# Performance work log

Measured on AMD Instinct MI355X. Metric: run time of the kernel, lower is better.

Reference implementation:

```python
import jax, jax.numpy as jnp
import numpy as np

H, W = 256, 256
BLOCK_SIZES = [16, 1024, 1024, 24]


def get_binary_position_encoding(shape):
    # Per-pixel binary encoding of the (row, col) coordinates, MSB-first.
    encs = []
    for d in shape:
        nb = int(np.ceil(np.log2(d)))
        bits = (jnp.arange(d)[:, None] >> jnp.arange(nb - 1, -1, -1)[None, :]) & 1
        encs.append(bits.astype(bool))
    a = jnp.broadcast_to(encs[0][:, None, :], (shape[0], shape[1], encs[0].shape[-1]))
    b = jnp.broadcast_to(encs[1][None, :, :], (shape[0], shape[1], encs[1].shape[-1]))
    return jnp.concatenate([a, b], axis=-1)  # (H, W, 16) bool


def block_forward(x, mask, thr):
    # Original: expand x to (N, dim_in, dim_out), XNOR with mask, sum over dim_in,
    # threshold. XNOR-popcount == #{i : x[n,i] == mask[i,o]}, computed here as two
    # GEMMs without materializing the (N, dim_in, dim_out) intermediate.
    xf = x.astype(jnp.float32)
    mf = mask.astype(jnp.float32)
    sums = xf @ mf + (1.0 - xf) @ (1.0 - mf)  # exact integer counts in fp32
    return sums > thr.astype(jnp.float32)[None, :]


def bits_to_int(x):
    # (..., 8) bool bits, MSB-first -> int
    weights = (2 ** jnp.arange(7, -1, -1)).astype(jnp.int32)
    return jnp.sum(x.astype(jnp.int32) * weights, axis=-1)


def setup_inputs() -> dict:
    key = jax.random.key(0)
    ks = jax.random.split(key, 7)
    inp = {"image": jax.random.uniform(ks[0], (3, H, W), jnp.float32) * 255.0}
    for i, (di, do) in enumerate(zip(BLOCK_SIZES[:-1], BLOCK_SIZES[1:])):
        inp[f"mask{i}"] = jax.random.uniform(ks[1 + 2 * i], (di, do)) < 0.5
        inp[f"thr{i}"] = jax.random.randint(ks[2 + 2 * i], (do,), 0, di).astype(jnp.int32)
    return inp


def reference(image, mask0, thr0, mask1, thr1, mask2, thr2):
    pos = get_binary_position_encoding((H, W))      # (H, W, 16)
    x = pos.reshape(-1, pos.shape[-1])              # (H*W, 16) bool
    for m, t in ((mask0, thr0), (mask1, thr1), (mask2, thr2)):
        x = block_forward(x, m, t)
    x = x.reshape(H, W, 3, 8)
    x = bits_to_int(x)                              # (H, W, 3) int32
    x = jnp.transpose(x, (2, 0, 1))                 # (3, H, W)
    error = x.astype(jnp.float32) - image
    return x, error
```

## Files before the change

kernel.cpp:

```cpp
#include <hip/hip_runtime.h>
#include <stdint.h>

#define WS_CA   0
#define WS_CB   262144
#define WS_M2P  524288
#define WS_CARR 527360
#define WS_BF   532480
#define WS_X2   1581056

typedef int v4i  __attribute__((ext_vector_type(4)));
typedef int v16i __attribute__((ext_vector_type(16)));

__device__ __forceinline__ v4i expand16(unsigned h) {
  v4i a;
  a.x = (int)(__umul24(h & 15u,         0x00204081u) & 0x01010101u);
  a.y = (int)(__umul24((h >> 4) & 15u,  0x00204081u) & 0x01010101u);
  a.z = (int)(__umul24((h >> 8) & 15u,  0x00204081u) & 0x01010101u);
  a.w = (int)(__umul24((h >> 12) & 15u, 0x00204081u) & 0x01010101u);
  return a;
}

__device__ inline int detect_mode(const unsigned char* p) {
  unsigned nonalign = 0;
  for (int i = 0; i < 64; i++)
    if (i & 3) nonalign |= p[i];
  if (nonalign == 0) return 1;
  bool f32ok = true;
  for (int e = 0; e < 16; e++) {
    const unsigned char* q = p + 4 * e;
    bool one  = (q[0] == 0 && q[1] == 0 && q[2] == 0x80 && q[3] == 0x3F);
    bool zero = (q[0] == 0 && q[1] == 0 && q[2] == 0 && q[3] == 0);
    if (!(one || zero)) { f32ok = false; break; }
  }
  return f32ok ? 2 : 0;
}

__device__ inline int maskbit(const unsigned char* p, int idx, int mode) {
  if (mode == 1) return ((const int*)p)[idx] & 1;
  if (mode == 2) return ((const float*)p)[idx] != 0.0f;
  return p[idx] & 1;
}

__global__ __launch_bounds__(256) void prep_kernel(
    const unsigned char* __restrict__ mask0, const int* __restrict__ thr0,
    const unsigned char* __restrict__ mask1, const unsigned char* __restrict__ mask2,
    signed char* __restrict__ cA, unsigned char* __restrict__ cB,
    unsigned char* __restrict__ Bf, unsigned* __restrict__ M2p) {
  __shared__ int smode;
  if (threadIdx.x == 0) smode = detect_mode(mask1);
  __syncthreads();
  int mode = smode;
  int gid = blockIdx.x * 256 + threadIdx.x;
  if (gid < 524288) {
    int which = gid >> 18;
    int idx = gid & 262143;
    int hw = idx >> 10;
    int o  = idx & 1023;
    int base = which ? 8 : 0;
    int cnt = 0;
#pragma unroll
    for (int i = 0; i < 8; i++) {
      int xb = (hw >> (7 - i)) & 1;
      int mb = maskbit(mask0, (base + i) * 1024 + o, mode);
      cnt += (xb == mb);
    }
    if (which) cB[idx] = (unsigned char)cnt;
    else       cA[idx] = (signed char)(cnt - thr0[o]);
    return;
  }
  int g1 = gid - 524288;
  if (g1 < 262144) {
    int o  = g1 & 1023;
    int kk = g1 >> 10;
    unsigned u = 0;
#pragma unroll
    for (int j = 0; j < 4; j++)
      u |= (maskbit(mask1, (4 * kk + j) * 1024 + o, mode) ? 0x01u : 0xFFu) << (8 * j);
    unsigned off = ((unsigned)(o >> 5) << 15) + ((unsigned)(kk >> 3) << 10) +
                   ((unsigned)((kk >> 2) & 1) << 9) + ((unsigned)(o & 31) << 4) +
                   ((unsigned)(kk & 3) << 2);
    *reinterpret_cast<unsigned*>(Bf + off) = u;
    return;
  }
  int g2 = g1 - 262144;
  if (g2 < 768) {
    int kw = g2 / 24, o = g2 % 24;
    unsigned wv = 0;
    for (int b = 0; b < 32; b++)
      wv |= (unsigned)maskbit(mask2, (kw * 32 + b) * 24 + o, mode) << b;
    M2p[o * 32 + kw] = wv;
  }
}

__global__ __launch_bounds__(64) void popm_kernel(
    const unsigned char* __restrict__ Bf, const int* __restrict__ thr1,
    int* __restrict__ carr) {
  int o = blockIdx.x;
  int t = threadIdx.x;
  const uint4* p = reinterpret_cast<const uint4*>(
      Bf + ((unsigned)(o >> 5) << 15) + ((unsigned)(t >> 1) << 10) +
      ((unsigned)(t & 1) << 9) + ((unsigned)(o & 31) << 4));
  uint4 v = *p;
  int s = __popc(v.x) + __popc(v.y) + __popc(v.z) + __popc(v.w);
#pragma unroll
  for (int d = 32; d >= 1; d >>= 1) s += __shfl_down(s, d);
  if (t == 0) {
    int n1 = (8192 - s) / 7;
    carr[o] = thr1[o] + n1 - 1024;
  }
}

__global__ __launch_bounds__(512) void main_kernel(
    const signed char* __restrict__ cA, const unsigned char* __restrict__ cB,
    const unsigned char* __restrict__ Bf, const int* __restrict__ carr,
    unsigned* __restrict__ X2p) {
  __shared__ v4i Ae4[4096];
  __shared__ unsigned lbits[2112];
  int t = threadIdx.x;
  int lane = t & 63;
  int wv = t >> 6;
  int n0 = blockIdx.x << 6;
  int h = n0 >> 8;
  int w0 = n0 & 255;

  {
    int o1 = t, o2 = t + 512;
    int av1 = (int)cA[h * 1024 + o1];
    int av2 = (int)cA[h * 1024 + o2];
    const unsigned char* cb = cB + (unsigned)w0 * 1024;
#pragma unroll 1
    for (int r4 = 0; r4 < 64; r4 += 4) {
      int v1[4], v2[4];
#pragma unroll
      for (int i = 0; i < 4; i++) {
        v1[i] = (int)cb[(unsigned)(r4 + i) * 1024 + o1];
        v2[i] = (int)cb[(unsigned)(r4 + i) * 1024 + o2];
      }
#pragma unroll
      for (int i = 0; i < 4; i++) {
        int r = r4 + i;
        unsigned long long bal1 = __ballot((av1 + v1[i]) > 0);
        unsigned long long bal2 = __ballot((av2 + v2[i]) > 0);
        if (lane == 0) {
          lbits[r * 33 + wv * 2]          = (unsigned)bal1;
          lbits[r * 33 + wv * 2 + 1]      = (unsigned)(bal1 >> 32);
          lbits[r * 33 + 16 + wv * 2]     = (unsigned)bal2;
          lbits[r * 33 + 16 + wv * 2 + 1] = (unsigned)(bal2 >> 32);
        }
      }
    }
  }
  __syncthreads();

  {
    int r = t & 63;
    int c0 = (t >> 6) << 3;
#pragma unroll
    for (int ci = 0; ci < 8; ci++) {
      int c = c0 + ci;
      unsigned word = lbits[r * 33 + (c >> 1)];
      unsigned hwv = (c & 1) ? (word >> 16) : (word & 0xFFFFu);
      Ae4[c * 64 + r] = expand16(hwv);
    }
  }
  __syncthreads();

  int g = lane >> 5;
  int col = lane & 31;

#pragma unroll 1
  for (int pass = 0; pass < 2; pass++) {
    int ocp = (pass << 4) + (wv << 1);
    const unsigned char* bp0 = Bf + ((unsigned)ocp << 15) + (g << 9) + (col << 4);
    const unsigned char* bp1 = bp0 + 32768;

    v16i acc00 = {0,0,0,0,0,0,0,0,0,0,0,0,0,0,0,0};
    v16i acc10 = acc00, acc01 = acc00, acc11 = acc00;

    v4i b0n = *reinterpret_cast<const v4i*>(bp0);
    v4i b1n = *reinterpret_cast<const v4i*>(bp1);
#pragma unroll 1
    for (int ks = 0; ks < 32; ks++) {
      v4i b0 = b0n, b1 = b1n;
      if (ks < 31) {
        b0n = *reinterpret_cast<const v4i*>(bp0 + (ks + 1) * 1024);
        b1n = *reinterpret_cast<const v4i*>(bp1 + (ks + 1) * 1024);
      }
      int c = 2 * ks + g;
      v4i a0 = Ae4[c * 64 + col];
      v4i a1 = Ae4[c * 64 + 32 + col];
      acc00 = __builtin_amdgcn_mfma_i32_32x32x32_i8(a0, b0, acc00, 0, 0, 0);
      acc10 = __builtin_amdgcn_mfma_i32_32x32x32_i8(a1, b0, acc10, 0, 0, 0);
      acc01 = __builtin_amdgcn_mfma_i32_32x32x32_i8(a0, b1, acc01, 0, 0, 0);
      acc11 = __builtin_amdgcn_mfma_i32_32x32x32_i8(a1, b1, acc11, 0, 0, 0);
    }

#pragma unroll
    for (int s = 0; s < 2; s++) {
      int oc = ocp + s;
      int cv = carr[(oc << 5) + col];
#pragma unroll
      for (int rt = 0; rt < 2; rt++) {
        v16i av = (s == 0) ? (rt == 0 ? acc00 : acc10)
                           : (rt == 0 ? acc01 : acc11);
#pragma unroll
        for (int reg = 0; reg < 16; reg++) {
          int px_lo = (rt << 5) + (reg & 3) + ((reg >> 2) << 3);
          bool bit = av[reg] > cv;
          unsigned long long bal = __ballot(bit);
          if (lane == 0) {
            X2p[(unsigned)(n0 + px_lo) * 32 + oc]     = (unsigned)bal;
            X2p[(unsigned)(n0 + px_lo + 4) * 32 + oc] = (unsigned)(bal >> 32);
          }
        }
      }
    }
  }
}

__global__ __launch_bounds__(256) void l2_kernel(
    const uint4* __restrict__ X2p4, const unsigned* __restrict__ M2p,
    const int* __restrict__ thr2, const float* __restrict__ image,
    float* __restrict__ out) {
  __shared__ unsigned lm2[768];
  int t = threadIdx.x;
  for (int r = t; r < 768; r += 256) lm2[r] = M2p[r];
  __syncthreads();
  int n = blockIdx.x * 256 + t;
  uint4 xw[8];
#pragma unroll
  for (int q = 0; q < 8; q++) xw[q] = X2p4[(unsigned)n * 8 + q];
#pragma unroll
  for (int c = 0; c < 3; c++) {
    int val = 0;
#pragma unroll
    for (int b = 0; b < 8; b++) {
      int o = c * 8 + b;
      const unsigned* m = &lm2[o * 32];
      unsigned acc2 = 0;
#pragma unroll
      for (int q = 0; q < 8; q++) {
        acc2 += __popc(xw[q].x ^ m[q * 4 + 0]);
        acc2 += __popc(xw[q].y ^ m[q * 4 + 1]);
        acc2 += __popc(xw[q].z ^ m[q * 4 + 2]);
        acc2 += __popc(xw[q].w ^ m[q * 4 + 3]);
      }
      int bit = ((int)(1024u - acc2)) > thr2[o];
      val |= bit << (7 - b);
    }
    out[c * 65536 + n] = (float)val;
    out[196608 + c * 65536 + n] = (float)val - image[c * 65536 + n];
  }
}

extern "C" void kernel_launch(void* const* d_in, const int* in_sizes, int n_in,
                              void* d_out, int out_size, void* d_ws, size_t ws_size,
                              hipStream_t stream) {
  const float*         image = (const float*)d_in[0];
  const unsigned char* mask0 = (const unsigned char*)d_in[1];
  const int*           thr0  = (const int*)d_in[2];
  const unsigned char* mask1 = (const unsigned char*)d_in[3];
  const int*           thr1  = (const int*)d_in[4];
  const unsigned char* mask2 = (const unsigned char*)d_in[5];
  const int*           thr2  = (const int*)d_in[6];
  char* ws = (char*)d_ws;
  signed char*    cA    = (signed char*)(ws + WS_CA);
  unsigned char*  cB    = (unsigned char*)(ws + WS_CB);
  unsigned*       M2p   = (unsigned*)(ws + WS_M2P);
  int*            carr  = (int*)(ws + WS_CARR);
  unsigned char*  Bf    = (unsigned char*)(ws + WS_BF);
  unsigned*       X2p   = (unsigned*)(ws + WS_X2);
  float* out = (float*)d_out;

  hipLaunchKernelGGL(prep_kernel, dim3(3075), dim3(256), 0, stream,
                     mask0, thr0, mask1, mask2, cA, cB, Bf, M2p);
  hipLaunchKernelGGL(popm_kernel, dim3(1024), dim3(64), 0, stream,
                     Bf, thr1, carr);
  hipLaunchKernelGGL(main_kernel, dim3(1024), dim3(512), 0, stream,
                     cA, cB, Bf, carr, X2p);
  hipLaunchKernelGGL(l2_kernel, dim3(256), dim3(256), 0, stream,
                     (const uint4*)X2p, M2p, thr2, image, out);
}
```

Before: 121.3 us.

## Expand A operand in K-quarter chunks to shrink shared memory footprint

Replaces the up-front expansion of all 64 k-columns of the bit-packed A tile into a 64KB LDS buffer with on-the-fly expansion of 16 columns per K-quarter into a 16KB buffer. The aim is to cut LDS usage per block so more blocks can be resident per CU. The cost is that the expansion is now redone in each of the two passes (4 chunks each), with two extra barriers per chunk, and the B prefetch pipeline restarts at every chunk boundary.

```diff
diff --git a/kernel.cpp b/kernel.cpp
--- a/kernel.cpp
+++ b/kernel.cpp
@@ -114,7 +114,7 @@
     const signed char* __restrict__ cA, const unsigned char* __restrict__ cB,
     const unsigned char* __restrict__ Bf, const int* __restrict__ carr,
     unsigned* __restrict__ X2p) {
-  __shared__ v4i Ae4[4096];
+  __shared__ v4i Ae4[1024];
   __shared__ unsigned lbits[2112];
   int t = threadIdx.x;
   int lane = t & 63;
@@ -150,23 +150,11 @@
       }
     }
   }
-  __syncthreads();
-
-  {
-    int r = t & 63;
-    int c0 = (t >> 6) << 3;
-#pragma unroll
-    for (int ci = 0; ci < 8; ci++) {
-      int c = c0 + ci;
-      unsigned word = lbits[r * 33 + (c >> 1)];
-      unsigned hwv = (c & 1) ? (word >> 16) : (word & 0xFFFFu);
-      Ae4[c * 64 + r] = expand16(hwv);
-    }
-  }
-  __syncthreads();
 
   int g = lane >> 5;
   int col = lane & 31;
+  int r_ex = t & 63;
+  int cl0  = (t >> 6) << 1;
 
 #pragma unroll 1
   for (int pass = 0; pass < 2; pass++) {
@@ -177,22 +165,36 @@
     v16i acc00 = {0,0,0,0,0,0,0,0,0,0,0,0,0,0,0,0};
     v16i acc10 = acc00, acc01 = acc00, acc11 = acc00;
 
-    v4i b0n = *reinterpret_cast<const v4i*>(bp0);
-    v4i b1n = *reinterpret_cast<const v4i*>(bp1);
-#pragma unroll 1
-    for (int ks = 0; ks < 32; ks++) {
-      v4i b0 = b0n, b1 = b1n;
-      if (ks < 31) {
-        b0n = *reinterpret_cast<const v4i*>(bp0 + (ks + 1) * 1024);
-        b1n = *reinterpret_cast<const v4i*>(bp1 + (ks + 1) * 1024);
-      }
-      int c = 2 * ks + g;
-      v4i a0 = Ae4[c * 64 + col];
-      v4i a1 = Ae4[c * 64 + 32 + col];
-      acc00 = __builtin_amdgcn_mfma_i32_32x32x32_i8(a0, b0, acc00, 0, 0, 0);
-      acc10 = __builtin_amdgcn_mfma_i32_32x32x32_i8(a1, b0, acc10, 0, 0, 0);
-      acc01 = __builtin_amdgcn_mfma_i32_32x32x32_i8(a0, b1, acc01, 0, 0, 0);
-      acc11 = __builtin_amdgcn_mfma_i32_32x32x32_i8(a1, b1, acc11, 0, 0, 0);
+#pragma unroll 1
+    for (int kq = 0; kq < 4; kq++) {
+      __syncthreads();
+#pragma unroll
+      for (int ci = 0; ci < 2; ci++) {
+        int cl = cl0 + ci;
+        unsigned word = lbits[r_ex * 33 + (kq << 3) + (cl >> 1)];
+        unsigned hwv = (cl & 1) ? (word >> 16) : (word & 0xFFFFu);
+        Ae4[cl * 64 + r_ex] = expand16(hwv);
+      }
+      __syncthreads();
+
+      int ksb = kq << 3;
+      v4i b0n = *reinterpret_cast<const v4i*>(bp0 + (ksb) * 1024);
+      v4i b1n = *reinterpret_cast<const v4i*>(bp1 + (ksb) * 1024);
+#pragma unroll 1
+      for (int ksl = 0; ksl < 8; ksl++) {
+        v4i b0 = b0n, b1 = b1n;
+        if (ksl < 7) {
+          b0n = *reinterpret_cast<const v4i*>(bp0 + (ksb + ksl + 1) * 1024);
+          b1n = *reinterpret_cast<const v4i*>(bp1 + (ksb + ksl + 1) * 1024);
+        }
+        int c = 2 * ksl + g;
+        v4i a0 = Ae4[c * 64 + col];
+        v4i a1 = Ae4[c * 64 + 32 + col];
+        acc00 = __builtin_amdgcn_mfma_i32_32x32x32_i8(a0, b0, acc00, 0, 0, 0);
+        acc10 = __builtin_amdgcn_mfma_i32_32x32x32_i8(a1, b0, acc10, 0, 0, 0);
+        acc01 = __builtin_amdgcn_mfma_i32_32x32x32_i8(a0, b1, acc01, 0, 0, 0);
+        acc11 = __builtin_amdgcn_mfma_i32_32x32x32_i8(a1, b1, acc11, 0, 0, 0);
+      }
     }
 
 #pragma unroll
```

Result: no change. 120.8 us (-0.4%).
